# Kernel tuning notes

Hardware: AMD Instinct MI355X
Metric: run time of the kernel (lower is better)

Reference implementation:

```python
import jax, jax.numpy as jnp
import numpy as np

D_MODEL = 1024
N_HEADS = 16
D_K = D_MODEL // N_HEADS
B, S = 2, 2048


def setup_inputs() -> dict:
    key = jax.random.key(0)
    ks = jax.random.split(key, 5)
    sc = 1.0 / np.sqrt(D_MODEL)
    return {
        "x": jax.random.normal(ks[0], (B, S, D_MODEL), dtype=jnp.float32),
        "W_qkv": jax.random.normal(ks[1], (D_MODEL, 3 * D_MODEL), dtype=jnp.float32) * sc,
        "b_qkv": jnp.zeros((3 * D_MODEL,), dtype=jnp.float32),
        "W_out": jax.random.normal(ks[2], (D_MODEL, D_MODEL), dtype=jnp.float32) * sc,
        "b_out": jnp.zeros((D_MODEL,), dtype=jnp.float32),
    }


def reference(x, W_qkv, b_qkv, W_out, b_out):
    Bb, Ss, _ = x.shape
    qkv = x @ W_qkv + b_qkv                     # [B,S,3*D]
    qkv = qkv.reshape(Bb, Ss, 3, N_HEADS, D_K)
    qkv = jnp.transpose(qkv, (2, 0, 3, 1, 4))   # [3,B,H,S,Dk]
    q, k, v = qkv[0], qkv[1], qkv[2]
    scale = jnp.asarray(np.sqrt(D_K), dtype=x.dtype)
    attn = jnp.einsum('bhsd,bhtd->bhst', q, k) / scale  # [B,H,S,S]
    attn = jax.nn.softmax(attn, axis=-1)
    out = jnp.einsum('bhst,bhtd->bhsd', attn, v)        # [B,H,S,Dk]
    out = jnp.transpose(out, (0, 2, 1, 3)).reshape(Bb, Ss, D_MODEL)
    return out @ W_out + b_out
```

## Files before the change

kernel.cpp:

```cpp
#include <hip/hip_runtime.h>

typedef __bf16 bf16x8 __attribute__((ext_vector_type(8)));
typedef __bf16 bf16x4 __attribute__((ext_vector_type(4)));
typedef float f32x4 __attribute__((ext_vector_type(4)));
typedef unsigned short u16;
typedef unsigned int u32;

__device__ __forceinline__ u16 f2bu(float f) {
  __bf16 h = (__bf16)f;
  return __builtin_bit_cast(u16, h);
}

__device__ __forceinline__ void gld16(const u16* g, const __bf16* lds) {
  __builtin_amdgcn_global_load_lds(
      (const __attribute__((address_space(1))) u32*)(uintptr_t)g,
      (__attribute__((address_space(3))) u32*)(u32)(uintptr_t)lds, 16, 0, 0);
}

__device__ __forceinline__ void tr_tile(const float* __restrict__ in, u16* __restrict__ out,
                                        int R, int C, int bx, int by, int tid) {
  __shared__ u16 t[64][65];
  int tx = tid & 63, ty = tid >> 6;
  int r0 = by * 64, c0 = bx * 64;
  for (int i = 0; i < 16; ++i)
    t[ty + i * 4][tx] = f2bu(in[(size_t)(r0 + ty + i * 4) * C + c0 + tx]);
  __syncthreads();
  for (int i = 0; i < 16; ++i)
    out[(size_t)(c0 + ty + i * 4) * R + r0 + tx] = t[tx][ty + i * 4];
}

__global__ __launch_bounds__(256) void prep(const float* __restrict__ Wqkv,
                                            u16* __restrict__ Wqkv_t,
                                            const float* __restrict__ Wout,
                                            u16* __restrict__ Wout_t,
                                            const float* __restrict__ x,
                                            u16* __restrict__ xb) {
  int id = blockIdx.x, tid = threadIdx.x;
  if (id < 768) {
    tr_tile(Wqkv, Wqkv_t, 1024, 3072, id % 48, id / 48, tid);
  } else if (id < 1024) {
    int id2 = id - 768;
    tr_tile(Wout, Wout_t, 1024, 1024, id2 % 16, id2 / 16, tid);
  } else {
    size_t i = ((size_t)(id - 1024) * 256 + tid) * 8;
    f32x4 a0 = *(const f32x4*)(x + i);
    f32x4 a1 = *(const f32x4*)(x + i + 4);
    bf16x8 v;
    for (int j = 0; j < 4; ++j) { v[j] = (__bf16)a0[j]; v[j + 4] = (__bf16)a1[j]; }
    *(bf16x8*)(xb + i) = v;
  }
}

__global__ __launch_bounds__(256) void transpose_v(const u16* __restrict__ V,
                                                   u16* __restrict__ Vt) {
  constexpr int S = 2048;
  __shared__ u16 t[64][65];
  int bh = blockIdx.y, s0 = blockIdx.x * 64;
  const u16* in = V + (size_t)bh * S * 64;
  u16* out = Vt + (size_t)bh * 64 * S;
  int tx = threadIdx.x & 63, ty = threadIdx.x >> 6;
  for (int i = 0; i < 16; ++i)
    t[ty + i * 4][tx] = in[(size_t)(s0 + ty + i * 4) * 64 + tx];
  __syncthreads();
  for (int i = 0; i < 16; ++i)
    out[(size_t)(ty + i * 4) * S + s0 + tx] = t[tx][ty + i * 4];
}

template <int MODE, int TM, int TN, int MT, int NT, int XM, int XN>
__global__ __launch_bounds__(256) void gemm_bt(const u16* __restrict__ A,
                                               const u16* __restrict__ Bt,
                                               const float* __restrict__ bias,
                                               void* __restrict__ O0v,
                                               u16* __restrict__ O1,
                                               u16* __restrict__ O2,
                                               int M, int N, int K) {
  constexpr int NI = TM / 32;
  constexpr int NJ = TN / 32;
  constexpr int AE = TM * 32;
  constexpr int BE = TN * 32;
  __shared__ __bf16 smem[2 * (AE + BE)];

  int tid = threadIdx.x;
  int w = tid >> 6, lane = tid & 63, quad = lane >> 4, l16 = lane & 15;
  int wr = w >> 1, wc = w & 1;

  int id = blockIdx.x;
  int xcd = id & 7, s0i = id >> 3;
  int mg = xcd % (MT / XM), ng = xcd / (MT / XM);
  int sm = s0i % XM, sn = s0i / XM;
  int m0 = (mg * XM + sm) * TM, n0 = (ng * XN + sn) * TN;

  int srow = w * 16 + (lane >> 2);
  int sch = (lane & 3) ^ ((lane >> 3) & 3);
  const u16* Ag = A + (size_t)(m0 + srow) * K + sch * 8;
  const u16* Bg = Bt + (size_t)(n0 + srow) * K + sch * 8;

  int swl = (quad ^ ((l16 >> 1) & 3)) << 3;

  f32x4 acc[NI][NJ] = {};

#define GLD_STEP(c, kk)                                                          \
  {                                                                              \
    for (int p = 0; p < TM / 64; ++p)                                            \
      gld16(Ag + (size_t)p * 64 * K + (kk), smem + (c) * (AE + BE) + w * 512 + p * 2048); \
    for (int p = 0; p < TN / 64; ++p)                                            \
      gld16(Bg + (size_t)p * 64 * K + (kk), smem + (c) * (AE + BE) + AE + w * 512 + p * 2048); \
  }

  GLD_STEP(0, 0);
  int NS = K / 32;
  for (int s = 0; s < NS; ++s) {
    int cur = s & 1;
    __syncthreads();
    if (s + 1 < NS) GLD_STEP(1 - cur, (s + 1) * 32);
    const __bf16* Asub = smem + cur * (AE + BE);
    const __bf16* Bsub = Asub + AE;
    bf16x8 af[NI], bfr[NJ];
    for (int i = 0; i < NI; ++i)
      af[i] = *(const bf16x8*)(Asub + (wr * (TM / 2) + i * 16 + l16) * 32 + swl);
    for (int j = 0; j < NJ; ++j)
      bfr[j] = *(const bf16x8*)(Bsub + (wc * (TN / 2) + j * 16 + l16) * 32 + swl);
    for (int i = 0; i < NI; ++i)
      for (int j = 0; j < NJ; ++j)
        acc[i][j] = __builtin_amdgcn_mfma_f32_16x16x32_bf16(af[i], bfr[j], acc[i][j], 0, 0, 0);
  }
#undef GLD_STEP

  if (MODE == 0) {
    float* O0 = (float*)O0v;
    for (int j = 0; j < NJ; ++j) {
      int n = n0 + wc * (TN / 2) + j * 16 + l16;
      float bv = bias[n];
      for (int i = 0; i < NI; ++i) {
        int mb = m0 + wr * (TM / 2) + i * 16 + quad * 4;
        for (int r = 0; r < 4; ++r)
          O0[(size_t)(mb + r) * N + n] = acc[i][j][r] + bv;
      }
    }
  } else {
    u16* O0 = (u16*)O0v;
    for (int j = 0; j < NJ; ++j) {
      int n = n0 + wc * (TN / 2) + j * 16 + l16;
      int which = n >> 10, rem = n & 1023, h = rem >> 6, d = rem & 63;
      float bv = bias[n];
      for (int i = 0; i < NI; ++i) {
        for (int r = 0; r < 4; ++r) {
          int m = m0 + wr * (TM / 2) + i * 16 + quad * 4 + r;
          int b = m >> 11, s = m & 2047;
          size_t o = (((size_t)(b * 16 + h)) * 2048 + s) * 64 + d;
          u16 val = f2bu(acc[i][j][r] + bv);
          if (which == 0) O0[o] = val;
          else if (which == 1) O1[o] = val;
          else O2[o] = val;
        }
      }
    }
  }
}

__global__ __launch_bounds__(256, 4) void flash_attn(const u16* __restrict__ Q,
                                                     const u16* __restrict__ K,
                                                     const u16* __restrict__ Vt,
                                                     u16* __restrict__ AO) {
  constexpr int S = 2048;
  __shared__ __bf16 Ks[2][64 * 64];
  __shared__ __bf16 Vs[2][64 * 64];
  __shared__ __bf16 Ps[4][16 * 64];

  int bh = blockIdx.x, qbase = blockIdx.y * 64;
  int tid = threadIdx.x, w = tid >> 6, lane = tid & 63, quad = lane >> 4, l16 = lane & 15;

  const u16* Qh = Q + (size_t)bh * S * 64;
  const u16* Kh = K + (size_t)bh * S * 64;
  const u16* Vh = Vt + (size_t)bh * 64 * S;

  int qrow = qbase + w * 16 + l16;
  bf16x8 qf0 = *(const bf16x8*)(Qh + (size_t)qrow * 64 + quad * 8);
  bf16x8 qf1 = *(const bf16x8*)(Qh + (size_t)qrow * 64 + 32 + quad * 8);

  int r0s = tid >> 3, b0s = tid & 7;
  int r1s = r0s + 32;
  int ko0 = r0s * 64 + ((b0s ^ (r0s & 7)) << 3);
  int ko1 = r1s * 64 + ((b0s ^ (r1s & 7)) << 3);

  bf16x8 kr0, kr1, vr0, vr1;
#define LOAD_TILE(tb)                                                   \
  {                                                                     \
    kr0 = *(const bf16x8*)(Kh + (size_t)((tb) + r0s) * 64 + b0s * 8);   \
    kr1 = *(const bf16x8*)(Kh + (size_t)((tb) + r1s) * 64 + b0s * 8);   \
    vr0 = *(const bf16x8*)(Vh + (size_t)r0s * S + (tb) + b0s * 8);      \
    vr1 = *(const bf16x8*)(Vh + (size_t)r1s * S + (tb) + b0s * 8);      \
  }
#define STORE_TILE(c)                                                   \
  {                                                                     \
    *(bf16x8*)(&Ks[c][ko0]) = kr0;                                      \
    *(bf16x8*)(&Ks[c][ko1]) = kr1;                                      \
    *(bf16x8*)(&Vs[c][ko0]) = vr0;                                      \
    *(bf16x8*)(&Vs[c][ko1]) = vr1;                                      \
  }

  LOAD_TILE(0);
  STORE_TILE(0);
  LOAD_TILE(64);
  __syncthreads();

  constexpr float C1 = 0.125f * 1.44269504f;
  constexpr float C0 = -12.0f * 1.44269504f;

  float l_part = 0.f;
  f32x4 o[4] = {};
  int xr = l16 & 7;
  int pw_base = l16 * 64 + (quad & 1) * 4;
  int pw_blk = quad >> 1;

  for (int it = 0; it < S / 64; ++it) {
    int c = it & 1;
    if (it + 1 < S / 64) STORE_TILE(1 - c);
    if (it + 2 < S / 64) LOAD_TILE((it + 2) * 64);

    for (int nt = 0; nt < 4; ++nt) {
      const __bf16* kb = &Ks[c][(nt * 16 + l16) * 64];
      bf16x8 kf0 = *(const bf16x8*)(kb + ((quad ^ xr) << 3));
      bf16x8 kf1 = *(const bf16x8*)(kb + (((quad + 4) ^ xr) << 3));
      f32x4 cc = {0.f, 0.f, 0.f, 0.f};
      cc = __builtin_amdgcn_mfma_f32_16x16x32_bf16(kf0, qf0, cc, 0, 0, 0);
      cc = __builtin_amdgcn_mfma_f32_16x16x32_bf16(kf1, qf1, cc, 0, 0, 0);
      bf16x4 pk;
      for (int r = 0; r < 4; ++r) {
        float p = __builtin_amdgcn_exp2f(fmaf(cc[r], C1, C0));
        l_part += p;
        pk[r] = (__bf16)p;
      }
      *(bf16x4*)(&Ps[w][pw_base + (((nt * 2 + pw_blk) ^ xr) << 3)]) = pk;
    }

    bf16x8 pf0 = *(const bf16x8*)(&Ps[w][l16 * 64 + ((quad ^ xr) << 3)]);
    bf16x8 pf1 = *(const bf16x8*)(&Ps[w][l16 * 64 + (((quad + 4) ^ xr) << 3)]);
    for (int dt = 0; dt < 4; ++dt) {
      const __bf16* vb = &Vs[c][(dt * 16 + l16) * 64];
      bf16x8 v0 = *(const bf16x8*)(vb + ((quad ^ xr) << 3));
      bf16x8 v1 = *(const bf16x8*)(vb + (((quad + 4) ^ xr) << 3));
      o[dt] = __builtin_amdgcn_mfma_f32_16x16x32_bf16(pf0, v0, o[dt], 0, 0, 0);
      o[dt] = __builtin_amdgcn_mfma_f32_16x16x32_bf16(pf1, v1, o[dt], 0, 0, 0);
    }
    __syncthreads();
  }
#undef LOAD_TILE
#undef STORE_TILE

  l_part += __shfl_xor(l_part, 16);
  l_part += __shfl_xor(l_part, 32);
  float linv[4];
  for (int r = 0; r < 4; ++r)
    linv[r] = 1.f / __shfl(l_part, quad * 4 + r);

  int b = bh >> 4, h = bh & 15;
  for (int dt = 0; dt < 4; ++dt)
    for (int r = 0; r < 4; ++r) {
      int s = qbase + w * 16 + quad * 4 + r;
      int d = dt * 16 + l16;
      AO[(((size_t)b * 2048 + s) * 16 + h) * 64 + d] = f2bu(o[dt][r] * linv[r]);
    }
}

extern "C" void kernel_launch(void* const* d_in, const int* in_sizes, int n_in,
                              void* d_out, int out_size, void* d_ws, size_t ws_size,
                              hipStream_t stream) {
  const float* x    = (const float*)d_in[0];
  const float* Wqkv = (const float*)d_in[1];
  const float* bqkv = (const float*)d_in[2];
  const float* Wout = (const float*)d_in[3];
  const float* bout = (const float*)d_in[4];
  float* out = (float*)d_out;

  u16* ws = (u16*)d_ws;
  size_t off = 0;
  u16* Wqkv_t = ws + off; off += (size_t)3072 * 1024;
  u16* Wout_t = ws + off; off += (size_t)1024 * 1024;
  u16* xb     = ws + off; off += (size_t)4096 * 1024;
  u16* Qb     = ws + off; off += (size_t)32 * 2048 * 64;
  u16* Kb     = ws + off; off += (size_t)32 * 2048 * 64;
  u16* Vb     = ws + off; off += (size_t)32 * 2048 * 64;
  u16* Vtb    = ws + off; off += (size_t)32 * 2048 * 64;
  u16* AO     = xb;

  prep<<<dim3(3072), 256, 0, stream>>>(Wqkv, Wqkv_t, Wout, Wout_t, x, xb);
  gemm_bt<1, 128, 128, 32, 24, 8, 12><<<dim3(768), 256, 0, stream>>>(
      xb, Wqkv_t, bqkv, (void*)Qb, Kb, Vb, 4096, 3072, 1024);
  transpose_v<<<dim3(32, 32), 256, 0, stream>>>(Vb, Vtb);
  flash_attn<<<dim3(32, 32), 256, 0, stream>>>(Qb, Kb, Vtb, AO);
  gemm_bt<0, 64, 64, 64, 16, 8, 16><<<dim3(1024), 256, 0, stream>>>(
      AO, Wout_t, bout, (void*)out, nullptr, nullptr, 4096, 1024, 1024);
}
```

Before: 188.1 us.

## Fuse V transpose into QKV GEMM epilogue via LDS-staged transposed store

Removes the separate transpose_v kernel and the intermediate V buffer. The QKV GEMM now stages its V output tiles through shared memory with a rotated layout to avoid bank conflicts, then writes them directly in [B,H,D,S] layout with 16-byte vector stores. Q and K outputs keep the scalar scattered store but choose the destination pointer per tile instead of per element. This saves one kernel launch and a full read and write of V, at the cost of extra syncs and LDS traffic in the V-producing GEMM blocks.

```diff
diff --git a/kernel.cpp b/kernel.cpp
--- a/kernel.cpp
+++ b/kernel.cpp
@@ -51,21 +51,6 @@
   }
 }
 
-__global__ __launch_bounds__(256) void transpose_v(const u16* __restrict__ V,
-                                                   u16* __restrict__ Vt) {
-  constexpr int S = 2048;
-  __shared__ u16 t[64][65];
-  int bh = blockIdx.y, s0 = blockIdx.x * 64;
-  const u16* in = V + (size_t)bh * S * 64;
-  u16* out = Vt + (size_t)bh * 64 * S;
-  int tx = threadIdx.x & 63, ty = threadIdx.x >> 6;
-  for (int i = 0; i < 16; ++i)
-    t[ty + i * 4][tx] = in[(size_t)(s0 + ty + i * 4) * 64 + tx];
-  __syncthreads();
-  for (int i = 0; i < 16; ++i)
-    out[(size_t)(ty + i * 4) * S + s0 + tx] = t[tx][ty + i * 4];
-}
-
 template <int MODE, int TM, int TN, int MT, int NT, int XM, int XN>
 __global__ __launch_bounds__(256) void gemm_bt(const u16* __restrict__ A,
                                                const u16* __restrict__ Bt,
@@ -126,7 +111,7 @@
   }
 #undef GLD_STEP
 
-  if (MODE == 0) {
+  if constexpr (MODE == 0) {
     float* O0 = (float*)O0v;
     for (int j = 0; j < NJ; ++j) {
       int n = n0 + wc * (TN / 2) + j * 16 + l16;
@@ -138,20 +123,43 @@
       }
     }
   } else {
-    u16* O0 = (u16*)O0v;
-    for (int j = 0; j < NJ; ++j) {
-      int n = n0 + wc * (TN / 2) + j * 16 + l16;
-      int which = n >> 10, rem = n & 1023, h = rem >> 6, d = rem & 63;
-      float bv = bias[n];
-      for (int i = 0; i < NI; ++i) {
-        for (int r = 0; r < 4; ++r) {
-          int m = m0 + wr * (TM / 2) + i * 16 + quad * 4 + r;
-          int b = m >> 11, s = m & 2047;
-          size_t o = (((size_t)(b * 16 + h)) * 2048 + s) * 64 + d;
-          u16 val = f2bu(acc[i][j][r] + bv);
-          if (which == 0) O0[o] = val;
-          else if (which == 1) O1[o] = val;
-          else O2[o] = val;
+    if (n0 >= 2048) {
+      __syncthreads();
+      __bf16* T = smem;
+      for (int j = 0; j < NJ; ++j) {
+        int nn = wc * (TN / 2) + j * 16 + l16;
+        float bv = bias[n0 + nn];
+        int rot = 8 * (nn & 15);
+        for (int i = 0; i < NI; ++i) {
+          int mmb = wr * (TM / 2) + i * 16 + quad * 4;
+          bf16x4 v4;
+          for (int r = 0; r < 4; ++r) v4[r] = (__bf16)(acc[i][j][r] + bv);
+          *(bf16x4*)(&T[nn * 128 + ((mmb + rot) & 127)]) = v4;
+        }
+      }
+      __syncthreads();
+      int b = m0 >> 11, s0m = m0 & 2047;
+      int row = tid & 127, half = tid >> 7;
+      int gn = n0 + row;
+      int h = (gn >> 6) & 15, d = gn & 63;
+      u16* dst = O2 + ((size_t)(b * 16 + h) * 64 + d) * 2048 + s0m + half * 64;
+      const __bf16* src = T + row * 128;
+      int rot = 8 * (row & 15);
+      for (int c = 0; c < 64; c += 8)
+        *(bf16x8*)(dst + c) = *(const bf16x8*)(src + ((half * 64 + c + rot) & 127));
+    } else {
+      u16* O0 = (u16*)O0v;
+      u16* Odst = (n0 >= 1024) ? O1 : O0;
+      for (int j = 0; j < NJ; ++j) {
+        int n = n0 + wc * (TN / 2) + j * 16 + l16;
+        int rem = n & 1023, h = rem >> 6, d = rem & 63;
+        float bv = bias[n];
+        for (int i = 0; i < NI; ++i) {
+          for (int r = 0; r < 4; ++r) {
+            int m = m0 + wr * (TM / 2) + i * 16 + quad * 4 + r;
+            int b = m >> 11, s = m & 2047;
+            Odst[(((size_t)(b * 16 + h)) * 2048 + s) * 64 + d] = f2bu(acc[i][j][r] + bv);
+          }
         }
       }
     }
@@ -280,14 +288,12 @@
   u16* xb     = ws + off; off += (size_t)4096 * 1024;
   u16* Qb     = ws + off; off += (size_t)32 * 2048 * 64;
   u16* Kb     = ws + off; off += (size_t)32 * 2048 * 64;
-  u16* Vb     = ws + off; off += (size_t)32 * 2048 * 64;
   u16* Vtb    = ws + off; off += (size_t)32 * 2048 * 64;
   u16* AO     = xb;
 
   prep<<<dim3(3072), 256, 0, stream>>>(Wqkv, Wqkv_t, Wout, Wout_t, x, xb);
   gemm_bt<1, 128, 128, 32, 24, 8, 12><<<dim3(768), 256, 0, stream>>>(
-      xb, Wqkv_t, bqkv, (void*)Qb, Kb, Vb, 4096, 3072, 1024);
-  transpose_v<<<dim3(32, 32), 256, 0, stream>>>(Vb, Vtb);
+      xb, Wqkv_t, bqkv, (void*)Qb, Kb, Vtb, 4096, 3072, 1024);
   flash_attn<<<dim3(32, 32), 256, 0, stream>>>(Qb, Kb, Vtb, AO);
   gemm_bt<0, 64, 64, 64, 16, 8, 16><<<dim3(1024), 256, 0, stream>>>(
       AO, Wout_t, bout, (void*)out, nullptr, nullptr, 4096, 1024, 1024);
```

Measured after the change: 190.9 us. About the same (+1.5%).
